# Kernel optimization log

Measured on AMD Instinct MI355X. Metric: run time of the kernel, lower is better.

The kernel has to match this reference:

```python
import jax, jax.numpy as jnp
import numpy as np


def setup_inputs() -> dict:
    key = jax.random.key(0)
    k1, k2, k3 = jax.random.split(key, 3)
    B, L, D, C = 4, 4096, 1024, 1
    x = jax.random.normal(k1, (B, L, D), dtype=jnp.float32)
    kernel = jax.random.normal(k2, (C, D, L), dtype=jnp.float32)
    Dskip = jax.random.normal(k3, (C, D), dtype=jnp.float32)
    return {"x": x, "kernel": kernel, "D": Dskip}


def reference(x, kernel, D):
    # x: [B, L, H]  kernel: [C, H, L]  D: [C, H]
    L = x.shape[1]
    n = 2 * L
    xt = jnp.transpose(x, (0, 2, 1))  # [B, H, L]
    # soft-threshold the kernel: relu(|k| - 0.1) * sign(k)
    k = jax.nn.relu(jnp.abs(kernel) - 0.1) * jnp.sign(kernel)
    k_f = jnp.fft.rfft(k, n=n)          # [C, H, n//2+1] complex
    x_f = jnp.fft.rfft(xt, n=n)         # [B, H, n//2+1] complex
    y_f = jnp.einsum('bhl,chl->bchl', x_f, k_f)
    y = jnp.fft.irfft(y_f, n=n)[..., :L]            # [B, C, H, L]
    y = y + jnp.einsum('bhl,ch->bchl', xt, D)        # skip term
    # rearrange 'b c h l -> b l (c h)'
    Bn, Cn, Hn, Ln = y.shape
    return jnp.transpose(y, (0, 3, 1, 2)).reshape(Bn, Ln, Cn * Hn)
```

## Files before the change

### kernel.cpp

```cpp
#include <hip/hip_runtime.h>


typedef __attribute__((ext_vector_type(8)))  short s16x8;
typedef __attribute__((ext_vector_type(16))) float f32x16;
typedef __attribute__((ext_vector_type(4)))  float f32x4;
typedef __attribute__((ext_vector_type(4)))  unsigned int u32x4;

constexpr int B_ = 4, L_ = 4096, H_ = 1024;
constexpr int PADX = 256;
constexpr int LX = L_ + PADX;
constexpr int LK = L_ + 32;
constexpr int ST = 256;
constexpr int NST = L_ / ST;

constexpr size_t XT_ELEMS = (size_t)B_ * H_ * LX;
constexpr size_t KR_ELEMS = (size_t)2 * H_ * LK;
constexpr size_t OT_ELEMS = (size_t)B_ * H_ * L_;
constexpr size_t WS_NEEDED = (XT_ELEMS + KR_ELEMS + OT_ELEMS) * sizeof(unsigned short);

constexpr int XS_ROW  = 4320;
constexpr int XS_BLKS = XS_ROW / 8;
constexpr int XS_US   = B_ * XS_ROW;
constexpr int KS_US   = 2 * LK;
constexpr int OAREA_DW = 4 * 132;
constexpr int SMEM_BYTES = XS_US * 2 + KS_US * 2 + 4 * OAREA_DW * 4;

constexpr int nHt = H_ / 64, nLt = L_ / 64;
constexpr int NXB = B_ * nLt * nHt;

__device__ __forceinline__ unsigned short f2bf(float f) {
    unsigned int u = __builtin_bit_cast(unsigned int, f);
    u += 0x7fffu + ((u >> 16) & 1u);
    return (unsigned short)(u >> 16);
}
__device__ __forceinline__ float bf2f(unsigned short u) {
    return __builtin_bit_cast(float, (unsigned int)u << 16);
}
__device__ __forceinline__ unsigned int sw16(unsigned int x) {
    return (x >> 16) | (x << 16);
}

__global__ __launch_bounds__(256)
void prep(const float* __restrict__ x, const float* __restrict__ kin,
          const float* __restrict__ Dk,
          unsigned short* __restrict__ xT, unsigned short* __restrict__ kR)
{
    __shared__ __align__(16) unsigned char pshm[16704];
    const int bid = blockIdx.x;
    if (bid < NXB) {
        float (*tile)[65] = (float (*)[65])pshm;
        const int b  = bid / (nLt * nHt);
        const int r0 = bid % (nLt * nHt);
        const int l0 = (r0 / nHt) * 64;
        const int h0 = (r0 % nHt) * 64;
        const int j  = threadIdx.x;
        const int h4 = j & 15;
        const int rg = j >> 4;
        #pragma unroll
        for (int it = 0; it < 4; ++it) {
            const int lr = rg + 16 * it;
            const f32x4 v = *(const f32x4*)(x + ((size_t)b * L_ + l0 + lr) * H_ + h0 + 4 * h4);
            tile[lr][4 * h4 + 0] = v.x; tile[lr][4 * h4 + 1] = v.y;
            tile[lr][4 * h4 + 2] = v.z; tile[lr][4 * h4 + 3] = v.w;
        }
        __syncthreads();
        const int lg = j & 7;
        #pragma unroll
        for (int pp = 0; pp < 2; ++pp) {
            const int hh = (j >> 3) + 32 * pp;
            unsigned int w0 = (unsigned int)f2bf(tile[8*lg+0][hh]) | ((unsigned int)f2bf(tile[8*lg+1][hh]) << 16);
            unsigned int w1 = (unsigned int)f2bf(tile[8*lg+2][hh]) | ((unsigned int)f2bf(tile[8*lg+3][hh]) << 16);
            unsigned int w2 = (unsigned int)f2bf(tile[8*lg+4][hh]) | ((unsigned int)f2bf(tile[8*lg+5][hh]) << 16);
            unsigned int w3 = (unsigned int)f2bf(tile[8*lg+6][hh]) | ((unsigned int)f2bf(tile[8*lg+7][hh]) << 16);
            const u32x4 v = {w0, w1, w2, w3};
            *(u32x4*)(xT + ((size_t)b * H_ + h0 + hh) * LX + PADX + l0 + 8 * lg) = v;
        }
        if (l0 == 0) {
            #pragma unroll
            for (int it = 0; it < 8; ++it) {
                const int idx = j + 256 * it;
                const int row = idx >> 5, off = idx & 31;
                const u32x4 z = {};
                *(u32x4*)(xT + ((size_t)b * H_ + h0 + row) * LX + off * 8) = z;
            }
        }
    } else {
        unsigned short* kb0 = (unsigned short*)pshm;
        unsigned short* kb1 = kb0 + 4144;
        const int h = bid - NXB;
        const int j = threadIdx.x;
        const float Dv = Dk[h];
        if (j < 40) { kb0[j] = 0; kb1[j] = 0; }
        const float* kh = kin + (size_t)h * L_;
        float vv[17];
        {
            const int l0 = 16 * j;
            float am = (j > 0) ? kh[l0 - 1] : 0.0f;
            vv[0] = copysignf(fmaxf(fabsf(am) - 0.1f, 0.0f), am);
            #pragma unroll
            for (int g = 0; g < 4; ++g) {
                const f32x4 a = *(const f32x4*)(kh + l0 + 4 * g);
                vv[1 + 4*g + 0] = copysignf(fmaxf(fabsf(a.x) - 0.1f, 0.0f), a.x);
                vv[1 + 4*g + 1] = copysignf(fmaxf(fabsf(a.y) - 0.1f, 0.0f), a.y);
                vv[1 + 4*g + 2] = copysignf(fmaxf(fabsf(a.z) - 0.1f, 0.0f), a.z);
                vv[1 + 4*g + 3] = copysignf(fmaxf(fabsf(a.w) - 0.1f, 0.0f), a.w);
            }
            if (j == 0) vv[1] += Dv;
        }
        {
            unsigned int d0[8], d1[8];
            #pragma unroll
            for (int g = 0; g < 8; ++g) {
                d0[g] = (unsigned int)f2bf(vv[1 + 2*g]) | ((unsigned int)f2bf(vv[2 + 2*g]) << 16);
                d1[g] = (unsigned int)f2bf(vv[0 + 2*g]) | ((unsigned int)f2bf(vv[1 + 2*g]) << 16);
            }
            u32x4* p0 = (u32x4*)(kb0 + 40 + 16 * j);
            u32x4* p1 = (u32x4*)(kb1 + 40 + 16 * j);
            p0[0] = u32x4{d0[0], d0[1], d0[2], d0[3]};
            p0[1] = u32x4{d0[4], d0[5], d0[6], d0[7]};
            p1[0] = u32x4{d1[0], d1[1], d1[2], d1[3]};
            p1[1] = u32x4{d1[4], d1[5], d1[6], d1[7]};
        }
        __syncthreads();
        for (int v = j; v < LK / 8; v += 256) {
            const u32x4 a0 = *(const u32x4*)(kb0 + 4128 - 8 * v);
            const u32x4 a1 = *(const u32x4*)(kb1 + 4128 - 8 * v);
            const u32x4 r0 = {sw16(a0.w), sw16(a0.z), sw16(a0.y), sw16(a0.x)};
            const u32x4 r1 = {sw16(a1.w), sw16(a1.z), sw16(a1.y), sw16(a1.x)};
            *(u32x4*)(kR + (size_t)h * LK + 8 * v) = r0;
            *(u32x4*)(kR + ((size_t)H_ + h) * LK + 8 * v) = r1;
        }
    }
}

#define BODY2(M1, M2)                                                        \
  {                                                                          \
    _Pragma("unroll")                                                        \
    for (int i = 0; i < 16; ++i) {                                           \
      u32x4 aw;                                                              \
      aw.x = abase[8*i+0]; aw.y = abase[8*i+1];                              \
      aw.z = abase[8*i+2]; aw.w = abase[8*i+3];                              \
      const s16x8 af = __builtin_bit_cast(s16x8, aw);                        \
      const int io = 32 * (i >> 1);                                          \
      __builtin_amdgcn_s_setprio(1);                                         \
      if (M2 >= 1) accH2 = __builtin_amdgcn_mfma_f32_32x32x16_bf16(          \
            af, held2[i], accH2, 0, 0, 0);                                   \
      if (M2 == 2) {                                                         \
        const s16x8 nf = *(const s16x8*)(((i & 1) ? p2b : p2a) + io);        \
        accL2 = __builtin_amdgcn_mfma_f32_32x32x16_bf16(af, nf, accL2,0,0,0);\
        held2[i] = nf;                                                       \
      }                                                                      \
      if (M1 >= 1) accH1 = __builtin_amdgcn_mfma_f32_32x32x16_bf16(          \
            af, held1[i], accH1, 0, 0, 0);                                   \
      if (M1 == 2) {                                                         \
        const s16x8 nf = *(const s16x8*)(((i & 1) ? p1b : p1a) + io);        \
        accL1 = __builtin_amdgcn_mfma_f32_32x32x16_bf16(af, nf, accL1,0,0,0);\
        held1[i] = nf;                                                       \
      }                                                                      \
      __builtin_amdgcn_s_setprio(0);                                         \
    }                                                                        \
    abase -= 128;                                                            \
    if (M1 == 2) { p1a -= 256; p1b -= 256; }                                 \
    if (M2 == 2) { p2a -= 256; p2b -= 256; }                                 \
  }

__global__ __launch_bounds__(256, 2)
void longconv_main(const unsigned short* __restrict__ xT,
                   const unsigned short* __restrict__ kR,
                   unsigned int* __restrict__ outT)
{
    __shared__ __align__(16) unsigned char smem[SMEM_BYTES];
    unsigned short* xs = (unsigned short*)smem;
    unsigned short* ks = (unsigned short*)(smem + (size_t)XS_US * 2);
    float* oarea = (float*)(smem + (size_t)XS_US * 2 + (size_t)KS_US * 2);

    const int h   = blockIdx.x;
    const int tid = threadIdx.x;

    constexpr int NXU = XS_BLKS * 4;
    constexpr int NKU = 2 * (LK / 8);
    for (int u = tid; u < NXU + NKU; u += 256) {
        if (u < NXU) {
            const int b = u / XS_BLKS, n = u - b * XS_BLKS;
            const u32x4 v = *(const u32x4*)(xT + ((size_t)b * H_ + h) * LX + 32 + n * 8);
            *(u32x4*)(xs + (size_t)b * XS_ROW + (size_t)(n ^ b) * 8) = v;
        } else {
            const int v2 = u - NXU;
            const int p = v2 / (LK / 8), i = v2 - p * (LK / 8);
            const u32x4 v = *(const u32x4*)(kR + ((size_t)p * H_ + h) * LK + i * 8);
            *(u32x4*)(ks + (size_t)p * LK + (size_t)i * 8) = v;
        }
    }
    __syncthreads();

    const int w  = tid >> 6, ln = tid & 63;
    const int m  = ln & 31,  q  = ln >> 5;
    const int t  = m >> 2,   b  = m & 3;
    const int s1 = 2 * w;
    const int s2 = 14 - 2 * w;

    const int base = 3871 - m + 8 * q;
    const int p    = base & 1;
    const unsigned int* abase = (const unsigned int*)(ks + p * LK + (base - p));
    const unsigned short* xrow = xs + (size_t)b * XS_ROW;
    const int nb = 4 * t + q;

    auto mk = [&](int si, int par) -> const unsigned short* {
        const int n = 32 * si + nb + 2 * par;
        return xrow + (size_t)((n ^ b) * 8);
    };
    const unsigned short *p1a = mk(s1 + 1, 0), *p1b = mk(s1 + 1, 1);
    const unsigned short *p2a = mk(s2 + 1, 0), *p2b = mk(s2 + 1, 1);

    s16x8 held1[16], held2[16];
    #pragma unroll
    for (int i = 0; i < 16; ++i) {
        const int io = 32 * (i >> 1);
        held1[i] = *(const s16x8*)(((i & 1) ? p1b : p1a) + io);
        held2[i] = *(const s16x8*)(((i & 1) ? p2b : p2a) + io);
    }
    p1a -= 256; p1b -= 256; p2a -= 256; p2b -= 256;

    f32x16 accL1 = {}, accH1 = {}, accL2 = {}, accH2 = {};

    for (int beta = 0; beta <= s1; ++beta) BODY2(2, 2);
    BODY2(1, 2);
    for (int beta = s1 + 2; beta <= s2; ++beta) BODY2(0, 2);
    BODY2(0, 1);

    float* ar = oarea + w * OAREA_DW;
    auto writeout = [&](const f32x16& acc, int si) {
        const int Ls = si * ST;
        #pragma unroll
        for (int rh = 0; rh < 2; ++rh) {
            #pragma unroll
            for (int rr2 = 0; rr2 < 2; ++rr2) {
                const int base4 = (8 * rr2 + 4 * q + 4 * t) & 15;
                f32x4 qd;
                qd.x = acc[4 * (2 * rh + rr2) + 0];
                qd.y = acc[4 * (2 * rh + rr2) + 1];
                qd.z = acc[4 * (2 * rh + rr2) + 2];
                qd.w = acc[4 * (2 * rh + rr2) + 3];
                *(f32x4*)(ar + b * 132 + 16 * t + base4) = qd;
            }
            __asm__ volatile("s_waitcnt lgkmcnt(0)" ::: "memory");
            #pragma unroll
            for (int bb = 0; bb < 4; ++bb) {
                const int g  = ln >> 3;
                const int uu = (2 * ln) & 15;
                const int s  = (uu + 4 * g) & 15;
                const float v0 = ar[bb * 132 + 16 * g + s];
                const float v1 = ar[bb * 132 + 16 * g + s + 1];
                const int l = 32 * g + 16 * rh + uu;
                const unsigned int pk =
                    (unsigned int)f2bf(v0) | ((unsigned int)f2bf(v1) << 16);
                outT[(((size_t)bb * H_ + h) * L_ + Ls + l) >> 1] = pk;
            }
            __asm__ volatile("s_waitcnt lgkmcnt(0)" ::: "memory");
        }
    };
    writeout(accL1, s1);
    writeout(accH1, s1 + 1);
    writeout(accL2, s2);
    writeout(accH2, s2 + 1);
}

__global__ __launch_bounds__(256)
void untranspose(const unsigned short* __restrict__ outT, float* __restrict__ out)
{
    __shared__ __align__(16) float tile[64][68];
    const int bid = blockIdx.x;
    const int b  = bid / (nLt * nHt);
    const int r0 = bid % (nLt * nHt);
    const int l0 = (r0 / nHt) * 64;
    const int h0 = (r0 % nHt) * 64;
    const int j  = threadIdx.x;
    const int lg = j & 7;
    #pragma unroll
    for (int pp = 0; pp < 2; ++pp) {
        const int hh = (j >> 3) + 32 * pp;
        const u32x4 v = *(const u32x4*)(outT + ((size_t)b * H_ + h0 + hh) * L_ + l0 + 8 * lg);
        const unsigned short* pu = (const unsigned short*)&v;
        #pragma unroll
        for (int i = 0; i < 8; ++i) {
            const int row = 8 * lg + i;
            tile[row][hh ^ (4 * lg)] = bf2f(pu[i]);
        }
    }
    __syncthreads();
    const int hg = j & 15;
    #pragma unroll
    for (int pp = 0; pp < 4; ++pp) {
        const int ll = (j >> 4) + 16 * pp;
        const f32x4 v = *(const f32x4*)(&tile[ll][4 * (hg ^ (ll >> 3))]);
        *(f32x4*)(out + ((size_t)b * L_ + l0 + ll) * H_ + h0 + 4 * hg) = v;
    }
}

constexpr int TLf = 32, Uf = 8, Wf = TLf + Uf - 1, HTf = 256;

__global__ __launch_bounds__(HTf)
void longconv_fp32(const float* __restrict__ x, const float* __restrict__ k,
                   const float* __restrict__ Dskip, float* __restrict__ out)
{
    const int h  = blockIdx.y * HTf + threadIdx.x;
    const int b  = blockIdx.z;
    const int lt = (int)gridDim.x - 1 - (int)blockIdx.x;
    const int L0 = lt * TLf;
    const float* __restrict__ xb = x + ((size_t)b * L_) * H_ + h;
    const float* __restrict__ kh = k + (size_t)h * L_;
    float acc[TLf]; float win[Wf];
    #pragma unroll
    for (int i = 0; i < Wf; ++i) {
        const int idx = L0 - (Uf - 1) + i;
        win[i] = (idx >= 0) ? xb[(size_t)idx * H_] : 0.0f;
    }
    const float Dv = Dskip[h];
    #pragma unroll
    for (int jj = 0; jj < TLf; ++jj) acc[jj] = win[jj + Uf - 1] * Dv;
    const int cmax = L0 / Uf + (TLf / Uf) - 1;
    for (int c = 0; c <= cmax; ++c) {
        float kr[Uf];
        #pragma unroll
        for (int u = 0; u < Uf; ++u) {
            const float a = kh[c * Uf + u];
            kr[u] = copysignf(fmaxf(fabsf(a) - 0.1f, 0.0f), a);
        }
        #pragma unroll
        for (int u = 0; u < Uf; ++u)
            #pragma unroll
            for (int jj = 0; jj < TLf; ++jj)
                acc[jj] = fmaf(kr[u], win[jj + (Uf - 1) - u], acc[jj]);
        if (c < cmax) {
            #pragma unroll
            for (int i = Wf - 1; i >= Uf; --i) win[i] = win[i - Uf];
            #pragma unroll
            for (int i = 0; i < Uf; ++i) {
                const int idx = L0 - (c + 1) * Uf - (Uf - 1) + i;
                win[i] = (idx >= 0) ? xb[(size_t)idx * H_] : 0.0f;
            }
        }
    }
    float* __restrict__ ob = out + ((size_t)b * L_ + L0) * H_ + h;
    #pragma unroll
    for (int jj = 0; jj < TLf; ++jj) ob[(size_t)jj * H_] = acc[jj];
}

extern "C" void kernel_launch(void* const* d_in, const int* in_sizes, int n_in,
                              void* d_out, int out_size, void* d_ws, size_t ws_size,
                              hipStream_t stream)
{
    const float* x  = (const float*)d_in[0];
    const float* k  = (const float*)d_in[1];
    const float* Dk = (const float*)d_in[2];
    float* out = (float*)d_out;

    if (ws_size >= WS_NEEDED) {
        unsigned short* xT = (unsigned short*)d_ws;
        unsigned short* kR = xT + XT_ELEMS;
        unsigned short* oT = kR + KR_ELEMS;
        prep<<<dim3(NXB + H_), dim3(256), 0, stream>>>(x, k, Dk, xT, kR);
        longconv_main<<<dim3(H_), dim3(256), 0, stream>>>(xT, kR, (unsigned int*)oT);
        untranspose<<<dim3(NXB), dim3(256), 0, stream>>>(oT, out);
    } else {
        dim3 grid(L_ / TLf, H_ / HTf, B_);
        longconv_fp32<<<grid, dim3(HTf), 0, stream>>>(x, k, Dk, out);
    }
}
```

Baseline: 215.8 us.

## Alias output staging into input LDS, raise occupancy, widen untranspose tiles

The output staging area in longconv_main now reuses the x/k shared-memory region after a barrier instead of having its own LDS allocation. This shrinks per-block LDS so launch bounds can request 3 blocks per SM instead of 2. The s_setprio hints around the MFMA loop are removed. Separately, untranspose now processes 128-row L tiles with all global loads issued up front, halving the block count. The risks are register spills under the tighter launch bound and the extra barrier.

```diff
diff --git a/kernel.cpp b/kernel.cpp
--- a/kernel.cpp
+++ b/kernel.cpp
@@ -23,10 +23,12 @@
 constexpr int XS_US   = B_ * XS_ROW;
 constexpr int KS_US   = 2 * LK;
 constexpr int OAREA_DW = 4 * 132;
-constexpr int SMEM_BYTES = XS_US * 2 + KS_US * 2 + 4 * OAREA_DW * 4;
+constexpr int SMEM_MAIN = XS_US * 2 + KS_US * 2;
 
 constexpr int nHt = H_ / 64, nLt = L_ / 64;
 constexpr int NXB = B_ * nLt * nHt;
+constexpr int nLt2 = L_ / 128;
+constexpr int NUT = B_ * nLt2 * nHt;
 
 __device__ __forceinline__ unsigned short f2bf(float f) {
     unsigned int u = __builtin_bit_cast(unsigned int, f);
@@ -142,7 +144,6 @@
       aw.z = abase[8*i+2]; aw.w = abase[8*i+3];                              \
       const s16x8 af = __builtin_bit_cast(s16x8, aw);                        \
       const int io = 32 * (i >> 1);                                          \
-      __builtin_amdgcn_s_setprio(1);                                         \
       if (M2 >= 1) accH2 = __builtin_amdgcn_mfma_f32_32x32x16_bf16(          \
             af, held2[i], accH2, 0, 0, 0);                                   \
       if (M2 == 2) {                                                         \
@@ -157,22 +158,20 @@
         accL1 = __builtin_amdgcn_mfma_f32_32x32x16_bf16(af, nf, accL1,0,0,0);\
         held1[i] = nf;                                                       \
       }                                                                      \
-      __builtin_amdgcn_s_setprio(0);                                         \
     }                                                                        \
     abase -= 128;                                                            \
     if (M1 == 2) { p1a -= 256; p1b -= 256; }                                 \
     if (M2 == 2) { p2a -= 256; p2b -= 256; }                                 \
   }
 
-__global__ __launch_bounds__(256, 2)
+__global__ __launch_bounds__(256, 3)
 void longconv_main(const unsigned short* __restrict__ xT,
                    const unsigned short* __restrict__ kR,
                    unsigned int* __restrict__ outT)
 {
-    __shared__ __align__(16) unsigned char smem[SMEM_BYTES];
+    __shared__ __align__(16) unsigned char smem[SMEM_MAIN];
     unsigned short* xs = (unsigned short*)smem;
     unsigned short* ks = (unsigned short*)(smem + (size_t)XS_US * 2);
-    float* oarea = (float*)(smem + (size_t)XS_US * 2 + (size_t)KS_US * 2);
 
     const int h   = blockIdx.x;
     const int tid = threadIdx.x;
@@ -228,6 +227,8 @@
     for (int beta = s1 + 2; beta <= s2; ++beta) BODY2(0, 2);
     BODY2(0, 1);
 
+    __syncthreads();
+    float* oarea = (float*)smem;
     float* ar = oarea + w * OAREA_DW;
     auto writeout = [&](const f32x16& acc, int si) {
         const int Ls = si * ST;
@@ -268,32 +269,42 @@
 __global__ __launch_bounds__(256)
 void untranspose(const unsigned short* __restrict__ outT, float* __restrict__ out)
 {
-    __shared__ __align__(16) float tile[64][68];
+    __shared__ __align__(16) float tile[128][68];
     const int bid = blockIdx.x;
-    const int b  = bid / (nLt * nHt);
-    const int r0 = bid % (nLt * nHt);
-    const int l0 = (r0 / nHt) * 64;
+    const int b  = bid / (nLt2 * nHt);
+    const int r0 = bid % (nLt2 * nHt);
+    const int l0 = (r0 / nHt) * 128;
     const int h0 = (r0 % nHt) * 64;
     const int j  = threadIdx.x;
     const int lg = j & 7;
-    #pragma unroll
-    for (int pp = 0; pp < 2; ++pp) {
-        const int hh = (j >> 3) + 32 * pp;
-        const u32x4 v = *(const u32x4*)(outT + ((size_t)b * H_ + h0 + hh) * L_ + l0 + 8 * lg);
-        const unsigned short* pu = (const unsigned short*)&v;
-        #pragma unroll
-        for (int i = 0; i < 8; ++i) {
-            const int row = 8 * lg + i;
-            tile[row][hh ^ (4 * lg)] = bf2f(pu[i]);
-        }
-    }
+    u32x4 v[2][2];
+    #pragma unroll
+    for (int tt = 0; tt < 2; ++tt)
+        #pragma unroll
+        for (int pp = 0; pp < 2; ++pp) {
+            const int hh = (j >> 3) + 32 * pp;
+            v[tt][pp] = *(const u32x4*)(outT + ((size_t)b * H_ + h0 + hh) * L_
+                                        + l0 + 64 * tt + 8 * lg);
+        }
+    #pragma unroll
+    for (int tt = 0; tt < 2; ++tt)
+        #pragma unroll
+        for (int pp = 0; pp < 2; ++pp) {
+            const int hh = (j >> 3) + 32 * pp;
+            const unsigned short* pu = (const unsigned short*)&v[tt][pp];
+            #pragma unroll
+            for (int i = 0; i < 8; ++i) {
+                const int row = 64 * tt + 8 * lg + i;
+                tile[row][hh ^ (4 * lg)] = bf2f(pu[i]);
+            }
+        }
     __syncthreads();
     const int hg = j & 15;
     #pragma unroll
-    for (int pp = 0; pp < 4; ++pp) {
-        const int ll = (j >> 4) + 16 * pp;
-        const f32x4 v = *(const f32x4*)(&tile[ll][4 * (hg ^ (ll >> 3))]);
-        *(f32x4*)(out + ((size_t)b * L_ + l0 + ll) * H_ + h0 + 4 * hg) = v;
+    for (int pz = 0; pz < 8; ++pz) {
+        const int ll = (j >> 4) + 16 * pz;
+        const f32x4 vv = *(const f32x4*)(&tile[ll][4 * (hg ^ ((ll >> 3) & 7))]);
+        *(f32x4*)(out + ((size_t)b * L_ + l0 + ll) * H_ + h0 + 4 * hg) = vv;
     }
 }
 
@@ -361,7 +372,7 @@
         unsigned short* oT = kR + KR_ELEMS;
         prep<<<dim3(NXB + H_), dim3(256), 0, stream>>>(x, k, Dk, xT, kR);
         longconv_main<<<dim3(H_), dim3(256), 0, stream>>>(xT, kR, (unsigned int*)oT);
-        untranspose<<<dim3(NXB), dim3(256), 0, stream>>>(oT, out);
+        untranspose<<<dim3(NUT), dim3(256), 0, stream>>>(oT, out);
     } else {
         dim3 grid(L_ / TLf, H_ / HTf, B_);
         longconv_fp32<<<grid, dim3(HTf), 0, stream>>>(x, k, Dk, out);
```

New measurement: 262.4 us. 21.6% more time.
